# Performance work log

Measured on AMD Instinct MI355X. Metric: run time of the kernel, lower is better.

Reference implementation:

```python
import jax, jax.numpy as jnp
import numpy as np

N, G = 10000, 200          # nodes, graphs
EL, EG = 160000, 500000    # local / global edges
S, V = 256, 64             # scalar / vector hidden dims
NA, NB = 16, 5             # atom types, bond types


def _lin(k, i, o):
    return (jax.random.normal(k, (i, o), jnp.float32) / np.sqrt(i))


def scatter_mean(vals, idx, num_segments):
    # vals: [N, ...]; idx: [N] int
    sums = jax.ops.segment_sum(vals, idx, num_segments=num_segments)
    cnt = jax.ops.segment_sum(jnp.ones((vals.shape[0],), vals.dtype), idx,
                              num_segments=num_segments)
    cnt = jnp.maximum(cnt, 1.0).reshape((-1,) + (1,) * (vals.ndim - 1))
    return sums / cnt


def calc_edge_attrs(edge_index, pos):
    src, tgt = edge_index[0], edge_index[1]
    r = pos[tgt] - pos[src]                      # [E,3]
    a = (pos[tgt] * pos[src]).sum(-1)            # [E]
    d = jnp.sqrt(jnp.clip((r ** 2).sum(-1), 1e-6))
    r_norm = r / d[:, None]
    return d, a, r_norm


def setup_inputs() -> dict:
    key = jax.random.key(0)
    ks = jax.random.split(key, 24)
    inp = {}
    inp["x"] = jax.random.normal(ks[0], (N, NA), jnp.float32)
    inp["t"] = jax.random.uniform(ks[1], (G, 1), jnp.float32)
    inp["pos"] = jax.random.normal(ks[2], (N, 3), jnp.float32)
    eil = jax.random.randint(ks[3], (2, EL), 0, N)
    eig = jax.random.randint(ks[4], (2, EG), 0, N)
    # avoid self-edges so edge distances are strictly positive (safe sqrt grads)
    eig = eig.at[1].set(jnp.where(eig[1] == eig[0], (eig[1] + 1) % N, eig[1]))
    eil = eil.at[1].set(jnp.where(eil[1] == eil[0], (eil[1] + 1) % N, eil[1]))
    inp["edge_index_local"] = eil
    inp["edge_index_global"] = eig
    inp["edge_attr_global"] = jax.random.normal(ks[5], (EG, NB), jnp.float32)
    inp["batch"] = jnp.sort(jax.random.randint(ks[6], (N,), 0, G))
    # learned parameters
    inp["W_time"], inp["b_time"] = _lin(ks[7], 1, S), jnp.zeros((S,), jnp.float32)
    inp["W_atom"], inp["b_atom"] = _lin(ks[8], NA, S), jnp.zeros((S,), jnp.float32)
    inp["W_at"], inp["b_at"] = _lin(ks[9], S, S), jnp.zeros((S,), jnp.float32)
    inp["W_shared"], inp["b_shared"] = _lin(ks[10], S, S), jnp.zeros((S,), jnp.float32)
    inp["W_b0"], inp["b_b0"] = _lin(ks[11], S + 1, S), jnp.zeros((S,), jnp.float32)
    inp["W_b1"], inp["b_b1"] = _lin(ks[12], S, 2 * NB), jnp.zeros((2 * NB,), jnp.float32)
    inp["W_coord"] = _lin(ks[13], V, 2)           # no bias
    inp["W_atoms"], inp["b_atoms"] = _lin(ks[14], S, 2 * NA), jnp.zeros((2 * NA,), jnp.float32)
    return inp


def reference(x, t, pos, edge_attr_global, W_time, b_time, W_atom, b_atom,
              W_at, b_at, W_shared, b_shared, W_b0, b_b0, W_b1, b_b1,
              W_coord, W_atoms, b_atoms,
              edge_index_local, edge_index_global, batch):
    # --- trunk: center positions, embed atoms + time ---
    pos = pos - scatter_mean(pos, batch, G)[batch]
    temb = t @ W_time + b_time                    # [G,S]
    tnode = temb[batch]                           # [N,S]
    s = x @ W_atom + b_atom
    s = (s + tnode) @ W_at + b_at                 # [N,S]
    # --- edge attrs (gather-compute pattern feeding the GNN) ---
    d_l, a_l, rn_l = calc_edge_attrs(edge_index_local, pos)
    d_g, a_g, rn_g = calc_edge_attrs(edge_index_global, pos)
    # GNN stand-in (identity on s, v, p): v initialized to zeros as in original
    v = jnp.zeros((N, 3, V), s.dtype)
    # --- prediction head ---
    s = jax.nn.silu(s @ W_shared + b_shared)
    j, i = edge_index_global[0], edge_index_global[1]
    d = jnp.sqrt(((pos[i] - pos[j]) ** 2).sum(-1, keepdims=True))  # [EG,1]
    edge = jnp.concatenate([s[i] + s[j], d], axis=-1)              # [EG,S+1]
    bonds = jax.nn.silu(edge @ W_b0 + b_b0) @ W_b1 + b_b1          # [EG,2*NB]
    bonds_pred, bonds_eps = bonds[:, :NB], bonds[:, NB:]
    coords = jnp.einsum('nkv,vo->nko', v, W_coord)                 # [N,3,2]
    coords = coords - scatter_mean(coords, batch, G)[batch]
    coords_eps0, coords_eps1 = coords[..., 0], coords[..., 1]      # [N,3]
    atoms = s @ W_atoms + b_atoms                                  # [N,2*NA]
    atoms_eps, atoms_pred = atoms[:, :NA], atoms[:, NA:]
    pos_c = pos - scatter_mean(pos, batch, G)[batch]
    coords_pred = pos_c + coords_eps1
    return (coords_pred, coords_eps0, atoms_pred, atoms_eps,
            bonds_pred, bonds_eps, d_l, rn_l, a_g, rn_g)
```

## Files before the change

### kernel.cpp

```cpp
#include <hip/hip_runtime.h>
#include <hip/hip_bf16.h>

typedef __hip_bfloat16 bf16;
typedef short bf16x8 __attribute__((ext_vector_type(8)));
typedef float f32x4 __attribute__((ext_vector_type(4)));
typedef float f32x2 __attribute__((ext_vector_type(2)));

#define N_NODES  10000
#define G_GRAPHS 200
#define EL_EDGES 160000
#define EG_EDGES 500000
#define S_DIM    256
#define APAD     264

#define BONDS_BLOCKS 15625
#define LOCAL_BLOCKS 625

#define WS_FLAG   0
#define WS_POSC   1024
#define WS_WD     31232
#define WS_BB0    31488
#define WS_BB1    34304
#define WS_WATOM  34560
#define WS_WTIME  38656
#define WS_BTIME  38912
#define WS_BATOM  39168
#define WS_BAT    39424
#define WS_BSH    39680
#define WS_BATOMS 39936
#define WS_T      40000
#define WS_X      40448
#define WT_AT     200448
#define WT_SH     233216
#define WT_B0     265984
#define WT_ATOMS  298752
#define WT_B1     302848
#define WS_H      304896
#define WS_END_FLOATS (WS_H + (N_NODES * S_DIM) / 4)

#define CHAN(S)    ((((S) >> 6) << 6) + (((S) & 3) << 4) + (((S) & 63) >> 2))
#define CHANINV(k) ((((k) >> 6) << 6) + (((k) & 15) << 2) + (((k) >> 4) & 3))

#define O_CPRED 0
#define O_CEPS  30000
#define O_APRED 60000
#define O_AEPS  220000
#define O_BPRED 380000
#define O_BEPS  2880000
#define O_DL    5380000
#define O_RNL   5540000
#define O_AG    6020000
#define O_RNG   6520000

__device__ __forceinline__ float b2f(bf16 v) { return __bfloat162float(v); }
__device__ __forceinline__ bf16  f2b(float v) { return __float2bfloat16(v); }
__device__ __forceinline__ unsigned short bbits(float v) {
    bf16 b = f2b(v);
    return *reinterpret_cast<unsigned short*>(&b);
}
__device__ __forceinline__ float ldin(const void* p, int idx, int isf32) {
    return isf32 ? ((const float*)p)[idx] : b2f(((const bf16*)p)[idx]);
}
__device__ __forceinline__ void stout(void* out, int f32o, size_t idx, float v) {
    if (f32o) ((float*)out)[idx] = v;
    else      ((bf16*)out)[idx]  = f2b(v);
}
__device__ __forceinline__ float silu(float p) {
    return p * __builtin_amdgcn_rcpf(1.0f + __expf(-p));
}
__device__ __forceinline__ int dtype_f32(const void* tt) {
    const unsigned short* q = (const unsigned short*)tt;
    int c = 0;
#pragma unroll
    for (int z = 0; z < 32; ++z) c += (q[z] >= 0x4000) ? 1 : 0;
    return c > 0;
}

__global__ void k_prep(const void* __restrict__ x, const void* __restrict__ tt,
                       const void* __restrict__ W_time, const void* __restrict__ b_time,
                       const void* __restrict__ W_atom, const void* __restrict__ b_atom,
                       const void* __restrict__ W_at, const void* __restrict__ b_at,
                       const void* __restrict__ W_shared, const void* __restrict__ b_shared,
                       const void* __restrict__ W_b0, const void* __restrict__ b_b0,
                       const void* __restrict__ W_b1, const void* __restrict__ b_b1,
                       const void* __restrict__ W_atoms, const void* __restrict__ b_atoms,
                       float* __restrict__ ws) {
    const int t = blockIdx.x * blockDim.x + threadIdx.x;
    const int f = dtype_f32(tt);
    if (t == 0) ws[WS_FLAG] = f ? 1.0f : 0.0f;
    if (t < 65536) {
        const int k = t >> 8, n = t & 255;
        ((unsigned short*)(ws + WT_AT))[n * 256 + k] = bbits(ldin(W_at, t, f));
        ((unsigned short*)(ws + WT_SH))[n * 256 + k] = bbits(ldin(W_shared, t, f));
        ((unsigned short*)(ws + WT_B0))[n * 256 + k] = bbits(ldin(W_b0, t, f));
    }
    if (t < 160000) ws[WS_X + t] = ldin(x, t, f);
    if (t < 8192) {
        const int k = t >> 5, n = t & 31;
        ((unsigned short*)(ws + WT_ATOMS))[n * 256 + k] = bbits(ldin(W_atoms, t, f));
    }
    if (t < 4096) ws[WS_WATOM + t] = ldin(W_atom, t, f);
    if (t < 2560) {
        const int k = t / 10, n = t - k * 10;
        ((unsigned short*)(ws + WT_B1))[n * 256 + CHANINV(k)] = bbits(ldin(W_b1, t, f));
    } else if (t < 4096) {
        ((unsigned short*)(ws + WT_B1))[t] = 0;
    }
    if (t < 256) {
        ws[WS_WD + t]    = ldin(W_b0, 65536 + CHAN(t), f);
        ws[WS_BB0 + t]   = ldin(b_b0, CHAN(t), f);
        ws[WS_WTIME + t] = ldin(W_time, t, f);
        ws[WS_BTIME + t] = ldin(b_time, t, f);
        ws[WS_BATOM + t] = ldin(b_atom, t, f);
        ws[WS_BAT + t]   = ldin(b_at, t, f);
        ws[WS_BSH + t]   = ldin(b_shared, t, f);
    }
    if (t < 200) ws[WS_T + t] = ldin(tt, t, f);
    if (t < 32)  ws[WS_BATOMS + t] = ldin(b_atoms, t, f);
    if (t < 16)  ws[WS_BB1 + t] = (t < 10) ? ldin(b_b1, t, f) : 0.0f;
}

__global__ void k_pos(const void* __restrict__ pos, const int* __restrict__ batch,
                      float* __restrict__ ws, void* __restrict__ out) {
    const int g = blockIdx.x;
    const int f32o = ws[WS_FLAG] != 0.0f;
    __shared__ int s_lo, s_hi;
    __shared__ float wsum[4][3];
    __shared__ float mean[3];
    if (threadIdx.x == 0) {
        int lo = 0, hi = N_NODES;
        while (lo < hi) { int m = (lo + hi) >> 1; if (batch[m] < g) lo = m + 1; else hi = m; }
        s_lo = lo;
        int lo2 = lo; hi = N_NODES;
        while (lo2 < hi) { int m = (lo2 + hi) >> 1; if (batch[m] < g + 1) lo2 = m + 1; else hi = m; }
        s_hi = lo2;
    }
    __syncthreads();
    const int lo = s_lo, hi = s_hi, cnt = hi - lo;
    float sx = 0.f, sy = 0.f, sz = 0.f;
    for (int n = lo + threadIdx.x; n < hi; n += 256) {
        sx += ldin(pos, n * 3 + 0, f32o);
        sy += ldin(pos, n * 3 + 1, f32o);
        sz += ldin(pos, n * 3 + 2, f32o);
    }
#pragma unroll
    for (int off = 32; off > 0; off >>= 1) {
        sx += __shfl_down(sx, off);
        sy += __shfl_down(sy, off);
        sz += __shfl_down(sz, off);
    }
    if ((threadIdx.x & 63) == 0) {
        wsum[threadIdx.x >> 6][0] = sx;
        wsum[threadIdx.x >> 6][1] = sy;
        wsum[threadIdx.x >> 6][2] = sz;
    }
    __syncthreads();
    if (threadIdx.x == 0) {
        float inv = 1.0f / (float)max(cnt, 1);
        mean[0] = (wsum[0][0] + wsum[1][0] + wsum[2][0] + wsum[3][0]) * inv;
        mean[1] = (wsum[0][1] + wsum[1][1] + wsum[2][1] + wsum[3][1]) * inv;
        mean[2] = (wsum[0][2] + wsum[1][2] + wsum[2][2] + wsum[3][2]) * inv;
    }
    __syncthreads();
    for (int n = lo + threadIdx.x; n < hi; n += 256) {
#pragma unroll
        for (int k = 0; k < 3; ++k) {
            float p = ldin(pos, n * 3 + k, f32o) - mean[k];
            ws[WS_POSC + n * 3 + k] = p;
            stout(out, f32o, O_CPRED + n * 3 + k, p);
            stout(out, f32o, O_CEPS + n * 3 + k, 0.0f);
        }
    }
}

__global__ __launch_bounds__(256) void k_node(
    const int* __restrict__ batch, const float* __restrict__ ws,
    unsigned int* __restrict__ h_out, void* __restrict__ out) {
    __shared__ unsigned short actA[16][APAD];
    __shared__ unsigned short actB[16][APAD];
    const int tid = threadIdx.x;
    const int wave = tid >> 6, lane = tid & 63;
    const int quad = lane >> 4, l16 = lane & 15;
    const int row0 = blockIdx.x * 16;

    {
        const int r = tid >> 4;
        const int c0 = (tid & 15) * 16;
        const int g = row0 + r;
        float tb = ws[WS_T + batch[g]];
        float xr[16];
#pragma unroll
        for (int k = 0; k < 16; ++k) xr[k] = ws[WS_X + g * 16 + k];
        for (int cc = 0; cc < 16; cc += 4) {
            const int c = c0 + cc;
            float a0 = ws[WS_BATOM + c + 0] + tb * ws[WS_WTIME + c + 0] + ws[WS_BTIME + c + 0];
            float a1 = ws[WS_BATOM + c + 1] + tb * ws[WS_WTIME + c + 1] + ws[WS_BTIME + c + 1];
            float a2 = ws[WS_BATOM + c + 2] + tb * ws[WS_WTIME + c + 2] + ws[WS_BTIME + c + 2];
            float a3 = ws[WS_BATOM + c + 3] + tb * ws[WS_WTIME + c + 3] + ws[WS_BTIME + c + 3];
#pragma unroll
            for (int k = 0; k < 16; ++k) {
                float4 w4 = *(const float4*)(ws + WS_WATOM + k * S_DIM + c);
                a0 += xr[k] * w4.x; a1 += xr[k] * w4.y;
                a2 += xr[k] * w4.z; a3 += xr[k] * w4.w;
            }
            actA[r][c + 0] = bbits(a0); actA[r][c + 1] = bbits(a1);
            actA[r][c + 2] = bbits(a2); actA[r][c + 3] = bbits(a3);
        }
    }
    __syncthreads();

    const unsigned short* wt_at = (const unsigned short*)(ws + WT_AT);
    const unsigned short* wt_sh = (const unsigned short*)(ws + WT_SH);
    const unsigned short* wt_b0 = (const unsigned short*)(ws + WT_B0);
    const unsigned short* wt_am = (const unsigned short*)(ws + WT_ATOMS);
    const int n0 = wave * 64;

    {
        f32x4 acc[4] = {};
        for (int kk = 0; kk < S_DIM; kk += 32) {
            const int k = kk + quad * 8;
            bf16x8 a = *(const bf16x8*)&actA[l16][k];
#pragma unroll
            for (int nt = 0; nt < 4; ++nt) {
                bf16x8 b = *(const bf16x8*)(wt_at + (size_t)(n0 + nt * 16 + l16) * S_DIM + k);
                acc[nt] = __builtin_amdgcn_mfma_f32_16x16x32_bf16(a, b, acc[nt], 0, 0, 0);
            }
        }
#pragma unroll
        for (int nt = 0; nt < 4; ++nt) {
            const int n = n0 + nt * 16 + l16;
            const float bv = ws[WS_BAT + n];
#pragma unroll
            for (int r = 0; r < 4; ++r)
                actB[quad * 4 + r][n] = bbits(acc[nt][r] + bv);
        }
    }
    __syncthreads();

    {
        f32x4 acc[4] = {};
        for (int kk = 0; kk < S_DIM; kk += 32) {
            const int k = kk + quad * 8;
            bf16x8 a = *(const bf16x8*)&actB[l16][k];
#pragma unroll
            for (int nt = 0; nt < 4; ++nt) {
                bf16x8 b = *(const bf16x8*)(wt_sh + (size_t)(n0 + nt * 16 + l16) * S_DIM + k);
                acc[nt] = __builtin_amdgcn_mfma_f32_16x16x32_bf16(a, b, acc[nt], 0, 0, 0);
            }
        }
        __syncthreads();
#pragma unroll
        for (int nt = 0; nt < 4; ++nt) {
            const int n = n0 + nt * 16 + l16;
            const float bv = ws[WS_BSH + n];
#pragma unroll
            for (int r = 0; r < 4; ++r)
                actA[quad * 4 + r][n] = bbits(silu(acc[nt][r] + bv));
        }
    }
    __syncthreads();

    {
        f32x4 acc[4] = {};
        for (int kk = 0; kk < S_DIM; kk += 32) {
            const int k = kk + quad * 8;
            bf16x8 a = *(const bf16x8*)&actA[l16][k];
#pragma unroll
            for (int nt = 0; nt < 4; ++nt) {
                bf16x8 b = *(const bf16x8*)(wt_b0 + (size_t)(n0 + nt * 16 + l16) * S_DIM + k);
                acc[nt] = __builtin_amdgcn_mfma_f32_16x16x32_bf16(a, b, acc[nt], 0, 0, 0);
            }
        }
#pragma unroll
        for (int r = 0; r < 4; ++r) {
            const int g = row0 + quad * 4 + r;
            int w = 0;
            w = __builtin_amdgcn_cvt_pk_fp8_f32(acc[0][r], acc[1][r], w, false);
            w = __builtin_amdgcn_cvt_pk_fp8_f32(acc[2][r], acc[3][r], w, true);
            h_out[(size_t)g * 64 + wave * 16 + l16] = (unsigned int)w;
        }
    }

    if (wave < 2) {
        f32x4 acc = {};
        const int n = wave * 16 + l16;
        for (int kk = 0; kk < S_DIM; kk += 32) {
            const int k = kk + quad * 8;
            bf16x8 a = *(const bf16x8*)&actA[l16][k];
            bf16x8 b = *(const bf16x8*)(wt_am + (size_t)n * S_DIM + k);
            acc = __builtin_amdgcn_mfma_f32_16x16x32_bf16(a, b, acc, 0, 0, 0);
        }
        const float bv = ws[WS_BATOMS + n];
        const int f32o = ws[WS_FLAG] != 0.0f;
#pragma unroll
        for (int r = 0; r < 4; ++r) {
            const int g = row0 + quad * 4 + r;
            float v = acc[r] + bv;
            if (n < 16) stout(out, f32o, O_AEPS + (size_t)g * 16 + n, v);
            else        stout(out, f32o, O_APRED + (size_t)g * 16 + (n - 16), v);
        }
    }
}

__global__ __launch_bounds__(256, 6) void k_edges(const int* __restrict__ eig,
                                                  const int* __restrict__ eil,
                                                  const float* __restrict__ ws,
                                                  const unsigned char* __restrict__ h,
                                                  void* __restrict__ out) {
    __shared__ unsigned char sm[2][32][272];
    const int f32o = ws[WS_FLAG] != 0.0f;

    if (blockIdx.x >= BONDS_BLOCKS) {
        const int e = (blockIdx.x - BONDS_BLOCKS) * 256 + threadIdx.x;
        const float* posc = ws + WS_POSC;
        const int s = eil[e];
        const int t = eil[EL_EDGES + e];
        float rx = posc[t * 3 + 0] - posc[s * 3 + 0];
        float ry = posc[t * 3 + 1] - posc[s * 3 + 1];
        float rz = posc[t * 3 + 2] - posc[s * 3 + 2];
        float dsq = rx * rx + ry * ry + rz * rz;
        float d = sqrtf(fmaxf(dsq, 1e-6f));
        float inv = 1.0f / d;
        stout(out, f32o, O_DL + e, d);
        stout(out, f32o, O_RNL + (size_t)e * 3 + 0, rx * inv);
        stout(out, f32o, O_RNL + (size_t)e * 3 + 1, ry * inv);
        stout(out, f32o, O_RNL + (size_t)e * 3 + 2, rz * inv);
        return;
    }

    const int wave = threadIdx.x >> 6, lane = threadIdx.x & 63;
    const int quad = lane >> 4, l16 = lane & 15;
    const int P = wave >> 1, sub = wave & 1;
    const int e0 = blockIdx.x * 32 + P * 16;

    uint4 tmp[4];
#pragma unroll
    for (int p = 0; p < 4; ++p) {
        const int r16 = p * 4 + quad;
        const int es = e0 + r16;
        const int node = sub ? eig[es] : eig[EG_EDGES + es];
        tmp[p] = *(const uint4*)(h + (size_t)node * 256 + l16 * 16);
    }
#pragma unroll
    for (int p = 0; p < 4; ++p) {
        const int row = sub * 16 + p * 4 + quad;
        *(uint4*)&sm[P][row][l16 * 16] = tmp[p];
    }

    if (sub == 0) {
        const int e = e0 + l16;
        const int j = eig[e];
        const int i = eig[EG_EDGES + e];
        const float* posc = ws + WS_POSC;
        float pix = posc[i * 3 + 0], piy = posc[i * 3 + 1], piz = posc[i * 3 + 2];
        float pjx = posc[j * 3 + 0], pjy = posc[j * 3 + 1], pjz = posc[j * 3 + 2];
        float rx = pix - pjx, ry = piy - pjy, rz = piz - pjz;
        float dsq = rx * rx + ry * ry + rz * rz;
        if (quad == 0) {
            float ag = pix * pjx + piy * pjy + piz * pjz;
            float inv = 1.0f / sqrtf(fmaxf(dsq, 1e-6f));
            stout(out, f32o, O_AG + e, ag);
            stout(out, f32o, O_RNG + (size_t)e * 3 + 0, rx * inv);
            stout(out, f32o, O_RNG + (size_t)e * 3 + 1, ry * inv);
            stout(out, f32o, O_RNG + (size_t)e * 3 + 2, rz * inv);
            *(float*)&sm[P][l16][256] = sqrtf(dsq);
        }
    }
    __syncthreads();

    const float d = *(const float*)&sm[P][l16][256];
    const float* __restrict__ wd  = ws + WS_WD;
    const float* __restrict__ bb0 = ws + WS_BB0;
    const unsigned short* __restrict__ wb1t = (const unsigned short*)(ws + WT_B1);

    const int kbase = sub * 128;
    f32x4 acc = {};
#pragma unroll
    for (int t = 0; t < 4; ++t) {
        const int k = kbase + t * 32 + quad * 8;
        uint2 uaw = *(const uint2*)&sm[P][l16][k];
        uint2 ubw = *(const uint2*)&sm[P][16 + l16][k];
        float4 wA = *(const float4*)(wd + k);
        float4 wB = *(const float4*)(wd + k + 4);
        float4 bA = *(const float4*)(bb0 + k);
        float4 bB = *(const float4*)(bb0 + k + 4);
        f32x2 a01 = __builtin_amdgcn_cvt_pk_f32_fp8((int)uaw.x, false);
        f32x2 a23 = __builtin_amdgcn_cvt_pk_f32_fp8((int)uaw.x, true);
        f32x2 a45 = __builtin_amdgcn_cvt_pk_f32_fp8((int)uaw.y, false);
        f32x2 a67 = __builtin_amdgcn_cvt_pk_f32_fp8((int)uaw.y, true);
        f32x2 b01 = __builtin_amdgcn_cvt_pk_f32_fp8((int)ubw.x, false);
        f32x2 b23 = __builtin_amdgcn_cvt_pk_f32_fp8((int)ubw.x, true);
        f32x2 b45 = __builtin_amdgcn_cvt_pk_f32_fp8((int)ubw.y, false);
        f32x2 b67 = __builtin_amdgcn_cvt_pk_f32_fp8((int)ubw.y, true);
        union { bf16x8 v; unsigned short s[8]; } af;
        af.s[0] = bbits(silu(a01.x + b01.x + fmaf(d, wA.x, bA.x)));
        af.s[1] = bbits(silu(a01.y + b01.y + fmaf(d, wA.y, bA.y)));
        af.s[2] = bbits(silu(a23.x + b23.x + fmaf(d, wA.z, bA.z)));
        af.s[3] = bbits(silu(a23.y + b23.y + fmaf(d, wA.w, bA.w)));
        af.s[4] = bbits(silu(a45.x + b45.x + fmaf(d, wB.x, bB.x)));
        af.s[5] = bbits(silu(a45.y + b45.y + fmaf(d, wB.y, bB.y)));
        af.s[6] = bbits(silu(a67.x + b67.x + fmaf(d, wB.z, bB.z)));
        af.s[7] = bbits(silu(a67.y + b67.y + fmaf(d, wB.w, bB.w)));
        bf16x8 bfr = *(const bf16x8*)(wb1t + (size_t)l16 * S_DIM + k);
        acc = __builtin_amdgcn_mfma_f32_16x16x32_bf16(af.v, bfr, acc, 0, 0, 0);
    }

    __syncthreads();
    f32x4* sc = (f32x4*)&sm[P][0][0];
    if (sub == 1) sc[lane] = acc;
    __syncthreads();
    if (sub == 0 && l16 < 10) {
        f32x4 o = sc[lane];
        const float bv = ws[WS_BB1 + l16];
#pragma unroll
        for (int r = 0; r < 4; ++r) {
            const int er = e0 + quad * 4 + r;
            float v = acc[r] + o[r] + bv;
            if (l16 < 5) stout(out, f32o, O_BPRED + (size_t)er * 5 + l16, v);
            else         stout(out, f32o, O_BEPS + (size_t)er * 5 + (l16 - 5), v);
        }
    }
}

extern "C" void kernel_launch(void* const* d_in, const int* in_sizes, int n_in,
                              void* d_out, int out_size, void* d_ws, size_t ws_size,
                              hipStream_t stream) {
    const void* x        = d_in[0];
    const void* t        = d_in[1];
    const void* pos      = d_in[2];
    const int*  eil      = (const int*)d_in[3];
    const int*  eig      = (const int*)d_in[4];
    const int*  batch    = (const int*)d_in[6];
    const void* W_time   = d_in[7];
    const void* b_time   = d_in[8];
    const void* W_atom   = d_in[9];
    const void* b_atom   = d_in[10];
    const void* W_at     = d_in[11];
    const void* b_at     = d_in[12];
    const void* W_shared = d_in[13];
    const void* b_shared = d_in[14];
    const void* W_b0     = d_in[15];
    const void* b_b0     = d_in[16];
    const void* W_b1     = d_in[17];
    const void* b_b1     = d_in[18];
    const void* W_atoms  = d_in[20];
    const void* b_atoms  = d_in[21];
    (void)in_sizes; (void)n_in; (void)out_size;

    const size_t NEED = (size_t)WS_END_FLOATS * sizeof(float);
    if (ws_size < NEED) return;

    float* ws = (float*)d_ws;
    unsigned int* hbuf = (unsigned int*)(ws + WS_H);

    k_prep<<<640, 256, 0, stream>>>(x, t, W_time, b_time, W_atom, b_atom,
                                    W_at, b_at, W_shared, b_shared, W_b0, b_b0,
                                    W_b1, b_b1, W_atoms, b_atoms, ws);
    k_pos<<<G_GRAPHS, 256, 0, stream>>>(pos, batch, ws, d_out);
    k_node<<<N_NODES / 16, 256, 0, stream>>>(batch, ws, hbuf, d_out);
    k_edges<<<BONDS_BLOCKS + LOCAL_BLOCKS, 256, 0, stream>>>(
        eig, eil, ws, (const unsigned char*)hbuf, d_out);
}
```

Before: 251.0 us.

## Process 64 node rows per block in k_node to reuse weight loads

The node MLP kernel now handles 64 rows per block instead of 16. Each weight fragment loaded from global memory feeds four MFMA row tiles, so weight traffic per node drops by about four times. A single shared activation buffer is reused in place, with an extra barrier. The change adds bounds checks for the ragged last block and uses a 4x4 accumulator array, which raises register pressure. It also launches only 157 blocks, which may underfill the GPU's CUs.

```diff
diff --git a/kernel.cpp b/kernel.cpp
--- a/kernel.cpp
+++ b/kernel.cpp
@@ -13,6 +13,8 @@
 #define S_DIM    256
 #define APAD     264
 
+#define NODE_M       64
+#define NODE_BLOCKS  157
 #define BONDS_BLOCKS 15625
 #define LOCAL_BLOCKS 625
 
@@ -173,38 +175,44 @@
     }
 }
 
-__global__ __launch_bounds__(256) void k_node(
+__global__ __launch_bounds__(256, 4) void k_node(
     const int* __restrict__ batch, const float* __restrict__ ws,
     unsigned int* __restrict__ h_out, void* __restrict__ out) {
-    __shared__ unsigned short actA[16][APAD];
-    __shared__ unsigned short actB[16][APAD];
+    __shared__ unsigned short act[NODE_M][APAD];
     const int tid = threadIdx.x;
     const int wave = tid >> 6, lane = tid & 63;
     const int quad = lane >> 4, l16 = lane & 15;
-    const int row0 = blockIdx.x * 16;
+    const int row0 = blockIdx.x * NODE_M;
 
     {
-        const int r = tid >> 4;
-        const int c0 = (tid & 15) * 16;
+        const int r = tid >> 2;
+        const int c0 = (tid & 3) * 64;
         const int g = row0 + r;
-        float tb = ws[WS_T + batch[g]];
-        float xr[16];
-#pragma unroll
-        for (int k = 0; k < 16; ++k) xr[k] = ws[WS_X + g * 16 + k];
-        for (int cc = 0; cc < 16; cc += 4) {
-            const int c = c0 + cc;
-            float a0 = ws[WS_BATOM + c + 0] + tb * ws[WS_WTIME + c + 0] + ws[WS_BTIME + c + 0];
-            float a1 = ws[WS_BATOM + c + 1] + tb * ws[WS_WTIME + c + 1] + ws[WS_BTIME + c + 1];
-            float a2 = ws[WS_BATOM + c + 2] + tb * ws[WS_WTIME + c + 2] + ws[WS_BTIME + c + 2];
-            float a3 = ws[WS_BATOM + c + 3] + tb * ws[WS_WTIME + c + 3] + ws[WS_BTIME + c + 3];
-#pragma unroll
-            for (int k = 0; k < 16; ++k) {
-                float4 w4 = *(const float4*)(ws + WS_WATOM + k * S_DIM + c);
-                a0 += xr[k] * w4.x; a1 += xr[k] * w4.y;
-                a2 += xr[k] * w4.z; a3 += xr[k] * w4.w;
-            }
-            actA[r][c + 0] = bbits(a0); actA[r][c + 1] = bbits(a1);
-            actA[r][c + 2] = bbits(a2); actA[r][c + 3] = bbits(a3);
+        if (g < N_NODES) {
+            float tb = ws[WS_T + batch[g]];
+            float xr[16];
+#pragma unroll
+            for (int k = 0; k < 16; ++k) xr[k] = ws[WS_X + g * 16 + k];
+            for (int cc = 0; cc < 64; cc += 4) {
+                const int c = c0 + cc;
+                float a0 = ws[WS_BATOM + c + 0] + tb * ws[WS_WTIME + c + 0] + ws[WS_BTIME + c + 0];
+                float a1 = ws[WS_BATOM + c + 1] + tb * ws[WS_WTIME + c + 1] + ws[WS_BTIME + c + 1];
+                float a2 = ws[WS_BATOM + c + 2] + tb * ws[WS_WTIME + c + 2] + ws[WS_BTIME + c + 2];
+                float a3 = ws[WS_BATOM + c + 3] + tb * ws[WS_WTIME + c + 3] + ws[WS_BTIME + c + 3];
+#pragma unroll
+                for (int k = 0; k < 16; ++k) {
+                    float4 w4 = *(const float4*)(ws + WS_WATOM + k * S_DIM + c);
+                    a0 += xr[k] * w4.x; a1 += xr[k] * w4.y;
+                    a2 += xr[k] * w4.z; a3 += xr[k] * w4.w;
+                }
+                act[r][c + 0] = bbits(a0); act[r][c + 1] = bbits(a1);
+                act[r][c + 2] = bbits(a2); act[r][c + 3] = bbits(a3);
+            }
+        } else {
+            for (int cc = 0; cc < 64; cc += 4) {
+                const int c = c0 + cc;
+                act[r][c] = 0; act[r][c + 1] = 0; act[r][c + 2] = 0; act[r][c + 3] = 0;
+            }
         }
     }
     __syncthreads();
@@ -216,36 +224,47 @@
     const int n0 = wave * 64;
 
     {
-        f32x4 acc[4] = {};
+        f32x4 acc[4][4] = {};
         for (int kk = 0; kk < S_DIM; kk += 32) {
             const int k = kk + quad * 8;
-            bf16x8 a = *(const bf16x8*)&actA[l16][k];
+            bf16x8 a[4];
+#pragma unroll
+            for (int mt = 0; mt < 4; ++mt) a[mt] = *(const bf16x8*)&act[mt * 16 + l16][k];
 #pragma unroll
             for (int nt = 0; nt < 4; ++nt) {
                 bf16x8 b = *(const bf16x8*)(wt_at + (size_t)(n0 + nt * 16 + l16) * S_DIM + k);
-                acc[nt] = __builtin_amdgcn_mfma_f32_16x16x32_bf16(a, b, acc[nt], 0, 0, 0);
-            }
-        }
+#pragma unroll
+                for (int mt = 0; mt < 4; ++mt)
+                    acc[mt][nt] = __builtin_amdgcn_mfma_f32_16x16x32_bf16(a[mt], b, acc[mt][nt], 0, 0, 0);
+            }
+        }
+        __syncthreads();
 #pragma unroll
         for (int nt = 0; nt < 4; ++nt) {
             const int n = n0 + nt * 16 + l16;
             const float bv = ws[WS_BAT + n];
 #pragma unroll
-            for (int r = 0; r < 4; ++r)
-                actB[quad * 4 + r][n] = bbits(acc[nt][r] + bv);
+            for (int mt = 0; mt < 4; ++mt)
+#pragma unroll
+                for (int r = 0; r < 4; ++r)
+                    act[mt * 16 + quad * 4 + r][n] = bbits(acc[mt][nt][r] + bv);
         }
     }
     __syncthreads();
 
     {
-        f32x4 acc[4] = {};
+        f32x4 acc[4][4] = {};
         for (int kk = 0; kk < S_DIM; kk += 32) {
             const int k = kk + quad * 8;
-            bf16x8 a = *(const bf16x8*)&actB[l16][k];
+            bf16x8 a[4];
+#pragma unroll
+            for (int mt = 0; mt < 4; ++mt) a[mt] = *(const bf16x8*)&act[mt * 16 + l16][k];
 #pragma unroll
             for (int nt = 0; nt < 4; ++nt) {
                 bf16x8 b = *(const bf16x8*)(wt_sh + (size_t)(n0 + nt * 16 + l16) * S_DIM + k);
-                acc[nt] = __builtin_amdgcn_mfma_f32_16x16x32_bf16(a, b, acc[nt], 0, 0, 0);
+#pragma unroll
+                for (int mt = 0; mt < 4; ++mt)
+                    acc[mt][nt] = __builtin_amdgcn_mfma_f32_16x16x32_bf16(a[mt], b, acc[mt][nt], 0, 0, 0);
             }
         }
         __syncthreads();
@@ -254,50 +273,68 @@
             const int n = n0 + nt * 16 + l16;
             const float bv = ws[WS_BSH + n];
 #pragma unroll
-            for (int r = 0; r < 4; ++r)
-                actA[quad * 4 + r][n] = bbits(silu(acc[nt][r] + bv));
+            for (int mt = 0; mt < 4; ++mt)
+#pragma unroll
+                for (int r = 0; r < 4; ++r)
+                    act[mt * 16 + quad * 4 + r][n] = bbits(silu(acc[mt][nt][r] + bv));
         }
     }
     __syncthreads();
 
     {
-        f32x4 acc[4] = {};
+        f32x4 acc[4][4] = {};
         for (int kk = 0; kk < S_DIM; kk += 32) {
             const int k = kk + quad * 8;
-            bf16x8 a = *(const bf16x8*)&actA[l16][k];
+            bf16x8 a[4];
+#pragma unroll
+            for (int mt = 0; mt < 4; ++mt) a[mt] = *(const bf16x8*)&act[mt * 16 + l16][k];
 #pragma unroll
             for (int nt = 0; nt < 4; ++nt) {
                 bf16x8 b = *(const bf16x8*)(wt_b0 + (size_t)(n0 + nt * 16 + l16) * S_DIM + k);
-                acc[nt] = __builtin_amdgcn_mfma_f32_16x16x32_bf16(a, b, acc[nt], 0, 0, 0);
-            }
-        }
-#pragma unroll
-        for (int r = 0; r < 4; ++r) {
-            const int g = row0 + quad * 4 + r;
-            int w = 0;
-            w = __builtin_amdgcn_cvt_pk_fp8_f32(acc[0][r], acc[1][r], w, false);
-            w = __builtin_amdgcn_cvt_pk_fp8_f32(acc[2][r], acc[3][r], w, true);
-            h_out[(size_t)g * 64 + wave * 16 + l16] = (unsigned int)w;
-        }
-    }
-
-    if (wave < 2) {
-        f32x4 acc = {};
-        const int n = wave * 16 + l16;
+#pragma unroll
+                for (int mt = 0; mt < 4; ++mt)
+                    acc[mt][nt] = __builtin_amdgcn_mfma_f32_16x16x32_bf16(a[mt], b, acc[mt][nt], 0, 0, 0);
+            }
+        }
+#pragma unroll
+        for (int mt = 0; mt < 4; ++mt)
+#pragma unroll
+            for (int r = 0; r < 4; ++r) {
+                const int g = row0 + mt * 16 + quad * 4 + r;
+                if (g < N_NODES) {
+                    int w = 0;
+                    w = __builtin_amdgcn_cvt_pk_fp8_f32(acc[mt][0][r], acc[mt][1][r], w, false);
+                    w = __builtin_amdgcn_cvt_pk_fp8_f32(acc[mt][2][r], acc[mt][3][r], w, true);
+                    h_out[(size_t)g * 64 + wave * 16 + l16] = (unsigned int)w;
+                }
+            }
+    }
+
+    {
+        f32x4 acc[2] = {};
         for (int kk = 0; kk < S_DIM; kk += 32) {
             const int k = kk + quad * 8;
-            bf16x8 a = *(const bf16x8*)&actA[l16][k];
-            bf16x8 b = *(const bf16x8*)(wt_am + (size_t)n * S_DIM + k);
-            acc = __builtin_amdgcn_mfma_f32_16x16x32_bf16(a, b, acc, 0, 0, 0);
-        }
-        const float bv = ws[WS_BATOMS + n];
+            bf16x8 a = *(const bf16x8*)&act[wave * 16 + l16][k];
+#pragma unroll
+            for (int hf = 0; hf < 2; ++hf) {
+                bf16x8 b = *(const bf16x8*)(wt_am + (size_t)(hf * 16 + l16) * S_DIM + k);
+                acc[hf] = __builtin_amdgcn_mfma_f32_16x16x32_bf16(a, b, acc[hf], 0, 0, 0);
+            }
+        }
         const int f32o = ws[WS_FLAG] != 0.0f;
 #pragma unroll
-        for (int r = 0; r < 4; ++r) {
-            const int g = row0 + quad * 4 + r;
-            float v = acc[r] + bv;
-            if (n < 16) stout(out, f32o, O_AEPS + (size_t)g * 16 + n, v);
-            else        stout(out, f32o, O_APRED + (size_t)g * 16 + (n - 16), v);
+        for (int hf = 0; hf < 2; ++hf) {
+            const int n = hf * 16 + l16;
+            const float bv = ws[WS_BATOMS + n];
+#pragma unroll
+            for (int r = 0; r < 4; ++r) {
+                const int g = row0 + wave * 16 + quad * 4 + r;
+                if (g < N_NODES) {
+                    float v = acc[hf][r] + bv;
+                    if (n < 16) stout(out, f32o, O_AEPS + (size_t)g * 16 + n, v);
+                    else        stout(out, f32o, O_APRED + (size_t)g * 16 + (n - 16), v);
+                }
+            }
         }
     }
 }
@@ -457,7 +494,7 @@
                                     W_at, b_at, W_shared, b_shared, W_b0, b_b0,
                                     W_b1, b_b1, W_atoms, b_atoms, ws);
     k_pos<<<G_GRAPHS, 256, 0, stream>>>(pos, batch, ws, d_out);
-    k_node<<<N_NODES / 16, 256, 0, stream>>>(batch, ws, hbuf, d_out);
+    k_node<<<NODE_BLOCKS, 256, 0, stream>>>(batch, ws, hbuf, d_out);
     k_edges<<<BONDS_BLOCKS + LOCAL_BLOCKS, 256, 0, stream>>>(
         eig, eil, ws, (const unsigned char*)hbuf, d_out);
 }
```

Measured after the change: 275.2 us. 1.1x slower.
